# Optimization experiments

Hardware: AMD Instinct MI355X
Metric: run time of the kernel (lower is better)

Reference implementation:

```python
import jax, jax.numpy as jnp
import numpy as np

N_QUBITS = 4
N_LAYERS = 3
B = 65536
EPS = 1e-5  # BatchNorm1d default eps

CNOT = jnp.array([[1, 0, 0, 0],
                  [0, 1, 0, 0],
                  [0, 0, 0, 1],
                  [0, 0, 1, 0]], dtype=jnp.complex64)


def _apply_1q(state, U, q):
    # state: [B, 2,2,2,2]; U: [2,2] (shared) or [B,2,2] (per-sample)
    s = jnp.moveaxis(state, 1 + q, -1)
    if U.ndim == 3:
        s = jnp.einsum('b...j,bij->b...i', s, U)
    else:
        s = jnp.einsum('...j,ij->...i', s, U)
    return jnp.moveaxis(s, -1, 1 + q)


def _apply_cnot(state, c, t):
    s = jnp.moveaxis(state, (1 + c, 1 + t), (-2, -1))
    shp = s.shape
    s = jnp.einsum('...j,ij->...i', s.reshape(shp[:-2] + (4,)), CNOT)
    return jnp.moveaxis(s.reshape(shp), (-2, -1), (1 + c, 1 + t))


def _rx_batched(theta):  # theta: [B] -> [B,2,2]
    c = jnp.cos(theta / 2).astype(jnp.complex64)
    s = (-1j * jnp.sin(theta / 2).astype(jnp.complex64))
    return jnp.stack([jnp.stack([c, s], -1), jnp.stack([s, c], -1)], -2)


def _ry(theta):  # scalar -> [2,2]
    c = jnp.cos(theta / 2).astype(jnp.complex64)
    s = jnp.sin(theta / 2).astype(jnp.complex64)
    return jnp.stack([jnp.stack([c, -s]), jnp.stack([s, c])])


def _rz(theta):  # scalar -> [2,2] diagonal
    e = jnp.exp(-1j * theta.astype(jnp.complex64) / 2)
    z = jnp.zeros_like(e)
    return jnp.stack([jnp.stack([e, z]), jnp.stack([z, jnp.conj(e)])])


def _circuit(angles, qparams):
    bsz = angles.shape[0]
    state = jnp.zeros((bsz, 2 ** N_QUBITS), jnp.complex64).at[:, 0].set(1.0)
    state = state.reshape((bsz,) + (2,) * N_QUBITS)
    for q in range(N_QUBITS):
        state = _apply_1q(state, _rx_batched(angles[:, q]), q)
    for l in range(N_LAYERS):
        for q in range(N_QUBITS):
            state = _apply_1q(state, _ry(qparams[l, q, 0]), q)
            state = _apply_1q(state, _rz(qparams[l, q, 1]), q)
        for q in range(N_QUBITS - 1):
            state = _apply_cnot(state, q, q + 1)
        state = _apply_cnot(state, N_QUBITS - 1, 0)
    probs = jnp.abs(state) ** 2  # [B,2,2,2,2]
    zs = []
    for q in range(N_QUBITS):
        axes = tuple(a for a in range(1, N_QUBITS + 1) if a != 1 + q)
        p = probs.sum(axes)  # [B,2]
        zs.append(p[:, 0] - p[:, 1])
    return jnp.stack(zs, -1)  # [B, n_qubits]


def setup_inputs() -> dict:
    key = jax.random.key(0)
    k1, k2, k3 = jax.random.split(key, 3)
    x = jax.random.normal(k1, (B, 1, 24, 24), dtype=jnp.float32)
    enc_w = 0.1 * jax.random.normal(k2, (N_QUBITS, 16), dtype=jnp.float32)
    enc_b = jnp.zeros((N_QUBITS,), jnp.float32)
    qparams = 0.01 * jax.random.normal(k3, (N_LAYERS, N_QUBITS, 3), dtype=jnp.float32)
    gamma = jnp.ones((N_QUBITS,), jnp.float32)
    beta = jnp.zeros((N_QUBITS,), jnp.float32)
    return {"x": x, "enc_w": enc_w, "enc_b": enc_b, "qparams": qparams,
            "gamma": gamma, "beta": beta}


def reference(x, enc_w, enc_b, qparams, gamma, beta):
    bsz = x.shape[0]
    # avg_pool2d(kernel=6, stride=6): [B,1,24,24] -> [B,1,4,4] -> [B,16]
    pooled = x.reshape(bsz, 1, 4, 6, 4, 6).mean((3, 5)).reshape(bsz, 16)
    angles = pooled @ enc_w.T + enc_b  # [B, n_qubits]
    out = _circuit(angles, qparams)    # [B, n_qubits]
    # BatchNorm1d (training mode: batch stats, biased var)
    mean = out.mean(0)
    var = out.var(0)
    return (out - mean) / jnp.sqrt(var + EPS) * gamma + beta
```

## Files before the change

kernel.cpp:

```cpp
#include <hip/hip_runtime.h>
#include <math.h>


#define BATCH 65536
#define SPW 8
#define MAIN_BLOCKS (BATCH / (4 * SPW))

__global__ __launch_bounds__(256) void qnat_precompute(const float* __restrict__ qp,
                                                       float* __restrict__ A,
                                                       double* __restrict__ acc) {
  __shared__ float Ur[16][17], Ui[16][17];
  const int tid = threadIdx.x;
  if (tid >= 64 && tid < 72) acc[tid - 64] = 0.0;
  if (tid < 16) {
    const int col = tid;
    float ur[16], ui[16];
#pragma unroll
    for (int i = 0; i < 16; i++) { ur[i] = (i == col) ? 1.f : 0.f; ui[i] = 0.f; }
#pragma unroll
    for (int l = 0; l < 3; l++) {
#pragma unroll
      for (int q = 0; q < 4; q++) {
        const int b = 3 - q;
        const float ty = qp[(l * 4 + q) * 3 + 0];
        const float tz = qp[(l * 4 + q) * 3 + 1];
        const float cy = cosf(0.5f * ty), sy = sinf(0.5f * ty);
#pragma unroll
        for (int i0 = 0; i0 < 16; i0++) {
          if (((i0 >> b) & 1) == 0) {
            const int i1 = i0 | (1 << b);
            const float r0 = ur[i0], m0 = ui[i0], r1 = ur[i1], m1 = ui[i1];
            ur[i0] = cy * r0 - sy * r1;  ui[i0] = cy * m0 - sy * m1;
            ur[i1] = sy * r0 + cy * r1;  ui[i1] = sy * m0 + cy * m1;
          }
        }
        const float cz = cosf(0.5f * tz), sz = sinf(0.5f * tz);
#pragma unroll
        for (int i0 = 0; i0 < 16; i0++) {
          if (((i0 >> b) & 1) == 0) {
            const int i1 = i0 | (1 << b);
            const float r0 = ur[i0], m0 = ui[i0], r1 = ur[i1], m1 = ui[i1];
            ur[i0] = cz * r0 + sz * m0;  ui[i0] = cz * m0 - sz * r0;
            ur[i1] = cz * r1 - sz * m1;  ui[i1] = cz * m1 + sz * r1;
          }
        }
      }
      const int cb[4] = {3, 2, 1, 0};
      const int tb[4] = {2, 1, 0, 3};
#pragma unroll
      for (int e = 0; e < 4; e++) {
#pragma unroll
        for (int i = 0; i < 16; i++) {
          if (((i >> cb[e]) & 1) && (((i >> tb[e]) & 1) == 0)) {
            const int j2 = i | (1 << tb[e]);
            float t0 = ur[i]; ur[i] = ur[j2]; ur[j2] = t0;
            float t1 = ui[i]; ui[i] = ui[j2]; ui[j2] = t1;
          }
        }
      }
    }
#pragma unroll
    for (int i = 0; i < 16; i++) { Ur[i][col] = ur[i]; Ui[i][col] = ui[i]; }
  }
  __syncthreads();
  const int j = tid >> 4, k = tid & 15;
#pragma unroll
  for (int q = 0; q < 4; q++) {
    const int b = 3 - q;
    float mr = 0.f, mi = 0.f;
#pragma unroll
    for (int i = 0; i < 16; i++) {
      const float z = ((i >> b) & 1) ? -1.f : 1.f;
      const float ar = Ur[i][j], ai = Ui[i][j], br = Ur[i][k], bi = Ui[i][k];
      mr += z * (ar * br + ai * bi);
      mi += z * (ar * bi - ai * br);
    }
    const int e = (__popc((unsigned)j) - __popc((unsigned)k)) & 3;
    const float re = (e == 0) ? mr : (e == 1) ? -mi : (e == 2) ? -mr : mi;
    A[(q << 8) + tid] = re;
  }
}

__global__ __launch_bounds__(256, 4) void qnat_main(const float* __restrict__ x,
                                                    const float* __restrict__ enc_w,
                                                    const float* __restrict__ enc_b,
                                                    const float* __restrict__ A,
                                                    float* __restrict__ out,
                                                    double* __restrict__ acc) {
  __shared__ float4 sW4[16];
  __shared__ double sAcc[4][4][2];
  const int tid = threadIdx.x;
  if (tid < 16) {
    const float inv36 = 1.0f / 36.0f;
    sW4[tid] = make_float4(enc_w[tid] * inv36, enc_w[16 + tid] * inv36,
                           enc_w[32 + tid] * inv36, enc_w[48 + tid] * inv36);
  }
  __syncthreads();

  const int wave = tid >> 6, lane = tid & 63;
  const int j = lane & 15;
  const int g = lane >> 4;

  float4 w[3][4];
#pragma unroll
  for (int t = 0; t < 3; t++) {
#pragma unroll
    for (int c = 0; c < 4; c++) {
      int p = t * 256 + 4 * lane + c;
      if (p > 575) p = 575;
      const int row = p / 24, colp = p - row * 24;
      const int fidx = (row / 6) * 4 + (colp / 6);
      w[t][c] = sW4[fidx];
    }
  }
  float Areg[16];
#pragma unroll
  for (int k = 0; k < 16; k++) Areg[k] = A[(g << 8) + (j << 4) + k];
  const float b0 = enc_b[0], b1 = enc_b[1], b2 = enc_b[2], b3 = enc_b[3];

  const int s0 = (blockIdx.x * 4 + wave) * SPW;
  double sd = 0.0, ssd = 0.0;

#define LOADS(S, V0, V1, V2)                                              \
  {                                                                       \
    const float4* p4 = (const float4*)(x + (size_t)(S) * 576);            \
    V0 = p4[lane];                                                        \
    V1 = p4[64 + lane];                                                   \
    V2 = (lane < 16) ? p4[128 + lane] : make_float4(0.f, 0.f, 0.f, 0.f);  \
  }

  float4 xv0, xv1, xv2;
  LOADS(s0, xv0, xv1, xv2);

  for (int i = 0; i < SPW; i++) {
    const int s = s0 + i;
    float4 xn0, xn1, xn2;
    if (i + 1 < SPW) LOADS(s + 1, xn0, xn1, xn2);

    float a0 = 0.f, a1 = 0.f, a2 = 0.f, a3 = 0.f;
#define ACC1(XS, T, C)                      \
    a0 = fmaf(XS, w[T][C].x, a0);           \
    a1 = fmaf(XS, w[T][C].y, a1);           \
    a2 = fmaf(XS, w[T][C].z, a2);           \
    a3 = fmaf(XS, w[T][C].w, a3);
#define ACC4(V, T) ACC1(V.x, T, 0) ACC1(V.y, T, 1) ACC1(V.z, T, 2) ACC1(V.w, T, 3)
    ACC4(xv0, 0) ACC4(xv1, 1) ACC4(xv2, 2)
#undef ACC4
#undef ACC1

#pragma unroll
    for (int off = 32; off >= 1; off >>= 1) {
      a0 += __shfl_xor(a0, off);
      a1 += __shfl_xor(a1, off);
      a2 += __shfl_xor(a2, off);
      a3 += __shfl_xor(a3, off);
    }
    const float th0 = a0 + b0, th1 = a1 + b1, th2 = a2 + b2, th3 = a3 + b3;
    float c0, s0_, c1, s1_, c2, s2_, c3, s3_;
    __sincosf(0.5f * th0, &s0_, &c0);
    __sincosf(0.5f * th1, &s1_, &c1);
    __sincosf(0.5f * th2, &s2_, &c2);
    __sincosf(0.5f * th3, &s3_, &c3);
    const float p01[4] = {c0 * c1, c0 * s1_, s0_ * c1, s0_ * s1_};
    const float p23[4] = {c2 * c3, c2 * s3_, s2_ * c3, s2_ * s3_};
    float inner = 0.f;
#pragma unroll
    for (int hi = 0; hi < 4; hi++) {
      float sh = 0.f;
#pragma unroll
      for (int lo = 0; lo < 4; lo++) sh = fmaf(Areg[4 * hi + lo], p23[lo], sh);
      inner = fmaf(p01[hi], sh, inner);
    }
    const float rj = ((j & 8) ? s0_ : c0) * ((j & 4) ? s1_ : c1) *
                     ((j & 2) ? s2_ : c2) * ((j & 1) ? s3_ : c3);
    float v = inner * rj;
    v += __shfl_xor(v, 1);
    v += __shfl_xor(v, 2);
    v += __shfl_xor(v, 4);
    v += __shfl_xor(v, 8);
    if (j == 0) {
      out[(size_t)s * 4 + g] = v;
      sd += (double)v;
      ssd = fma((double)v, (double)v, ssd);
    }

    if (i + 1 < SPW) { xv0 = xn0; xv1 = xn1; xv2 = xn2; }
  }
#undef LOADS

  if (j == 0) { sAcc[wave][g][0] = sd; sAcc[wave][g][1] = ssd; }
  __syncthreads();
  if (tid < 8) {
    const int q = tid & 3, m = tid >> 2;
    const double t = sAcc[0][q][m] + sAcc[1][q][m] + sAcc[2][q][m] + sAcc[3][q][m];
    atomicAdd(&acc[m * 4 + q], t);
  }
}

__global__ __launch_bounds__(256) void qnat_norm(float* __restrict__ out,
                                                 const double* __restrict__ acc,
                                                 const float* __restrict__ gamma,
                                                 const float* __restrict__ beta) {
  __shared__ float sMean[4], sScale[4], sBeta[4];
  const int tid = threadIdx.x;
  if (tid < 4) {
    const double n = (double)BATCH;
    const double mean = acc[tid] / n;
    const double var = acc[4 + tid] / n - mean * mean;
    const double inv = 1.0 / sqrt(var + 1e-5);
    sMean[tid] = (float)mean;
    sScale[tid] = (float)(gamma[tid] * inv);
    sBeta[tid] = beta[tid];
  }
  __syncthreads();
  const size_t i = (size_t)blockIdx.x * 256 + tid;
  float4 v = ((const float4*)out)[i];
  v.x = (v.x - sMean[0]) * sScale[0] + sBeta[0];
  v.y = (v.y - sMean[1]) * sScale[1] + sBeta[1];
  v.z = (v.z - sMean[2]) * sScale[2] + sBeta[2];
  v.w = (v.w - sMean[3]) * sScale[3] + sBeta[3];
  ((float4*)out)[i] = v;
}

extern "C" void kernel_launch(void* const* d_in, const int* in_sizes, int n_in,
                              void* d_out, int out_size, void* d_ws, size_t ws_size,
                              hipStream_t stream) {
  const float* x       = (const float*)d_in[0];
  const float* enc_w   = (const float*)d_in[1];
  const float* enc_b   = (const float*)d_in[2];
  const float* qparams = (const float*)d_in[3];
  const float* gamma   = (const float*)d_in[4];
  const float* beta    = (const float*)d_in[5];
  float* out = (float*)d_out;

  float* A = (float*)d_ws;
  double* acc = (double*)((char*)d_ws + 4096);

  qnat_precompute<<<1, 256, 0, stream>>>(qparams, A, acc);
  qnat_main<<<MAIN_BLOCKS, 256, 0, stream>>>(x, enc_w, enc_b, A, out, acc);
  qnat_norm<<<256, 256, 0, stream>>>(out, acc, gamma, beta);
}
```

Baseline: 58.04 us.

## Pre-sum adjacent pixel pairs and use transpose-reduce for encoder angles

Each lane's four pixels always sit in two pooling windows, so adjacent pairs are summed first, which halves the FMAs per float4 and the number of weight registers. The four-way butterfly reduction over 64 lanes becomes a transpose-style reduction: the first two shuffle stages exchange different accumulators, so each lane ends up holding one qubit's angle. After that one sincos runs per lane instead of four, and the sin/cos values are broadcast with eight extra shuffles. The change cuts shuffle count and transcendental work but adds select logic and broadcast shuffles; it relies on the pixel layout grouping pairs inside a single pooling window.

```diff
diff --git a/kernel.cpp b/kernel.cpp
--- a/kernel.cpp
+++ b/kernel.cpp
@@ -100,23 +100,22 @@
   const int wave = tid >> 6, lane = tid & 63;
   const int j = lane & 15;
   const int g = lane >> 4;
-
-  float4 w[3][4];
+  const bool bit0 = lane & 1, bit1 = lane & 2;
+
+  float4 wXr[3], wYr[3];
 #pragma unroll
   for (int t = 0; t < 3; t++) {
-#pragma unroll
-    for (int c = 0; c < 4; c++) {
-      int p = t * 256 + 4 * lane + c;
-      if (p > 575) p = 575;
-      const int row = p / 24, colp = p - row * 24;
-      const int fidx = (row / 6) * 4 + (colp / 6);
-      w[t][c] = sW4[fidx];
-    }
+    int p0 = t * 256 + 4 * lane;
+    if (p0 > 572) p0 = 572;
+    const int row = p0 / 24, col = p0 - row * 24;
+    const int rr = (row / 6) * 4;
+    wXr[t] = sW4[rr + col / 6];
+    wYr[t] = sW4[rr + (col + 3) / 6];
   }
   float Areg[16];
 #pragma unroll
   for (int k = 0; k < 16; k++) Areg[k] = A[(g << 8) + (j << 4) + k];
-  const float b0 = enc_b[0], b1 = enc_b[1], b2 = enc_b[2], b3 = enc_b[3];
+  const float bq = enc_b[lane & 3];
 
   const int s0 = (blockIdx.x * 4 + wave) * SPW;
   double sd = 0.0, ssd = 0.0;
@@ -138,29 +137,38 @@
     if (i + 1 < SPW) LOADS(s + 1, xn0, xn1, xn2);
 
     float a0 = 0.f, a1 = 0.f, a2 = 0.f, a3 = 0.f;
-#define ACC1(XS, T, C)                      \
-    a0 = fmaf(XS, w[T][C].x, a0);           \
-    a1 = fmaf(XS, w[T][C].y, a1);           \
-    a2 = fmaf(XS, w[T][C].z, a2);           \
-    a3 = fmaf(XS, w[T][C].w, a3);
-#define ACC4(V, T) ACC1(V.x, T, 0) ACC1(V.y, T, 1) ACC1(V.z, T, 2) ACC1(V.w, T, 3)
-    ACC4(xv0, 0) ACC4(xv1, 1) ACC4(xv2, 2)
-#undef ACC4
-#undef ACC1
-
-#pragma unroll
-    for (int off = 32; off >= 1; off >>= 1) {
-      a0 += __shfl_xor(a0, off);
-      a1 += __shfl_xor(a1, off);
-      a2 += __shfl_xor(a2, off);
-      a3 += __shfl_xor(a3, off);
-    }
-    const float th0 = a0 + b0, th1 = a1 + b1, th2 = a2 + b2, th3 = a3 + b3;
-    float c0, s0_, c1, s1_, c2, s2_, c3, s3_;
-    __sincosf(0.5f * th0, &s0_, &c0);
-    __sincosf(0.5f * th1, &s1_, &c1);
-    __sincosf(0.5f * th2, &s2_, &c2);
-    __sincosf(0.5f * th3, &s3_, &c3);
+#define ACCT(V, T)                                           \
+    {                                                        \
+      const float h0 = V.x + V.y, h1 = V.z + V.w;            \
+      a0 = fmaf(h0, wXr[T].x, fmaf(h1, wYr[T].x, a0));       \
+      a1 = fmaf(h0, wXr[T].y, fmaf(h1, wYr[T].y, a1));       \
+      a2 = fmaf(h0, wXr[T].z, fmaf(h1, wYr[T].z, a2));       \
+      a3 = fmaf(h0, wXr[T].w, fmaf(h1, wYr[T].w, a3));       \
+    }
+    ACCT(xv0, 0) ACCT(xv1, 1) ACCT(xv2, 2)
+#undef ACCT
+
+    float snd, rcv;
+    snd = bit0 ? a0 : a1; rcv = __shfl_xor(snd, 1);
+    float Af = (bit0 ? a1 : a0) + rcv;
+    snd = bit0 ? a2 : a3; rcv = __shfl_xor(snd, 1);
+    float Bf = (bit0 ? a3 : a2) + rcv;
+    snd = bit1 ? Af : Bf; rcv = __shfl_xor(snd, 2);
+    float Cf = (bit1 ? Bf : Af) + rcv;
+    Cf += __shfl_xor(Cf, 4);
+    Cf += __shfl_xor(Cf, 8);
+    Cf += __shfl_xor(Cf, 16);
+    Cf += __shfl_xor(Cf, 32);
+
+    float sm, cm;
+    __sincosf(0.5f * (Cf + bq), &sm, &cm);
+
+    const int base = lane & ~3;
+    const float c0 = __shfl(cm, base + 0), s0_ = __shfl(sm, base + 0);
+    const float c1 = __shfl(cm, base + 1), s1_ = __shfl(sm, base + 1);
+    const float c2 = __shfl(cm, base + 2), s2_ = __shfl(sm, base + 2);
+    const float c3 = __shfl(cm, base + 3), s3_ = __shfl(sm, base + 3);
+
     const float p01[4] = {c0 * c1, c0 * s1_, s0_ * c1, s0_ * s1_};
     const float p23[4] = {c2 * c3, c2 * s3_, s2_ * c3, s2_ * s3_};
     float inner = 0.f;
```

After: 59.76 us. 3.0% more time.
